# Kernel optimization log

Hardware: AMD Instinct MI355X
Metric: run time of the kernel (lower is better)

Reference implementation:

```python
import jax, jax.numpy as jnp
import numpy as np

N_NODES = 102400
N_EDGES = 1638400
NUM_GRAPHS = 128
IN_DIM = 128
HID = 128
OUT_DIM = 2
NUM_LAYERS = 3
BN_EPS = 1e-5


def setup_inputs() -> dict:
    key = jax.random.key(0)
    ks = jax.random.split(key, 12)
    x = jax.random.normal(ks[0], (N_NODES, IN_DIM), dtype=jnp.float32)
    edge_index = jax.random.randint(ks[1], (2, N_EDGES), 0, N_NODES, dtype=jnp.int64)
    # 128 graphs of 800 nodes each, sorted segment ids
    batch = jnp.repeat(jnp.arange(NUM_GRAPHS, dtype=jnp.int64), N_NODES // NUM_GRAPHS)
    s = 1.0 / np.sqrt(HID)
    W_conv = jax.random.uniform(ks[2], (NUM_LAYERS, HID, HID), jnp.float32, -s, s)
    b_conv = jnp.zeros((NUM_LAYERS, HID), jnp.float32)
    gamma = jnp.ones((NUM_LAYERS, HID), jnp.float32)
    beta = jnp.zeros((NUM_LAYERS, HID), jnp.float32)
    s2 = 1.0 / np.sqrt(3 * HID)
    W_mp1 = jax.random.uniform(ks[3], (3 * HID, 3 * HID), jnp.float32, -s2, s2)
    b_mp1 = jax.random.uniform(ks[4], (3 * HID,), jnp.float32, -s2, s2)
    W_mp2 = jax.random.uniform(ks[5], (3 * HID, OUT_DIM), jnp.float32, -s2, s2)
    b_mp2 = jax.random.uniform(ks[6], (OUT_DIM,), jnp.float32, -s2, s2)
    return {"x": x, "edge_index": edge_index, "batch": batch,
            "W_conv": W_conv, "b_conv": b_conv, "gamma": gamma, "beta": beta,
            "W_mp1": W_mp1, "b_mp1": b_mp1, "W_mp2": W_mp2, "b_mp2": b_mp2}


def _gcn_norm(edge_index, n):
    # add self loops, symmetric normalization: norm_e = deg^-1/2[src] * deg^-1/2[dst]
    loop = jnp.arange(n, dtype=edge_index.dtype)
    src = jnp.concatenate([edge_index[0], loop])
    dst = jnp.concatenate([edge_index[1], loop])
    deg = jax.ops.segment_sum(jnp.ones_like(dst, dtype=jnp.float32), dst, num_segments=n)
    dinv = jnp.where(deg > 0, jax.lax.rsqrt(deg), 0.0)
    return src, dst, dinv[src] * dinv[dst]


def reference(x, edge_index, batch, W_conv, b_conv, gamma, beta, W_mp1, b_mp1, W_mp2, b_mp2):
    n = x.shape[0]
    src, dst, norm = _gcn_norm(edge_index, n)
    for i in range(NUM_LAYERS):
        h = x @ W_conv[i]                                    # [N, HID]
        h = jax.ops.segment_sum(h[src] * norm[:, None], dst, num_segments=n) + b_conv[i]
        h = jax.nn.relu(h)
        mu = jnp.mean(h, axis=0)
        var = jnp.var(h, axis=0)                             # biased, as torch BN
        x = (h - mu) * jax.lax.rsqrt(var + BN_EPS) * gamma[i] + beta[i]
        # dropout p=0.0 -> no-op
    # readout: max pool, mean pool, first-node gather
    x1 = jax.ops.segment_max(x, batch, num_segments=NUM_GRAPHS)
    cnt = jax.ops.segment_sum(jnp.ones((n,), jnp.float32), batch, num_segments=NUM_GRAPHS)
    x2 = jax.ops.segment_sum(x, batch, num_segments=NUM_GRAPHS) / cnt[:, None]
    first_idx = jnp.searchsorted(batch, jnp.arange(NUM_GRAPHS, dtype=batch.dtype))
    x3 = x[first_idx]
    g = jnp.concatenate([x1, x2, x3], axis=1)                # [B, 3*HID]
    g = (g @ W_mp1 + b_mp1) @ W_mp2 + b_mp2
    return jax.nn.log_softmax(g, axis=1)
```

## Files before the change

kernel.cpp:

```cpp
#include <hip/hip_runtime.h>
#include <hip/hip_bf16.h>
#include <cstdint>

#define N_NODESC  102400
#define N_EDGESC  1638400
#define NUM_GRAPHS 128
#define NPG       800
#define HID       128
#define BN_EPS    1e-5f

#define NFINE 1600
#define NCOARSE 25
#define ROUND 2048

typedef short short8 __attribute__((ext_vector_type(8)));
typedef float f32x4  __attribute__((ext_vector_type(4)));
typedef unsigned long long u64;

__device__ __forceinline__ unsigned short f2bf(float f){
    union { __hip_bfloat16 h; unsigned short u; } cv;
    cv.h = __float2bfloat16(f);
    return cv.u;
}
__device__ __forceinline__ float bflo(unsigned int g){ return __uint_as_float(g << 16); }
__device__ __forceinline__ float bfhi(unsigned int g){ return __uint_as_float(g & 0xffff0000u); }
__device__ __forceinline__ float bfu(unsigned short u){ return __uint_as_float(((unsigned int)u) << 16); }

__global__ __launch_bounds__(256) void k_h1(const int* __restrict__ ei, int* __restrict__ fineCount){
    __shared__ int h[NFINE];
    int t = threadIdx.x;
    for (int i = t; i < NFINE; i += 256) h[i] = 0;
    __syncthreads();
    for (int e = blockIdx.x*256 + t; e < N_EDGESC; e += gridDim.x*256){
        int d = __builtin_nontemporal_load(&ei[N_EDGESC + e]);
        atomicAdd(&h[d >> 6], 1);
    }
    __syncthreads();
    for (int i = t; i < NFINE; i += 256) if (h[i]) atomicAdd(&fineCount[i], h[i]);
}

__global__ __launch_bounds__(256) void k_scanF(const int* __restrict__ fineCount, int* __restrict__ fineBase,
                                               int* __restrict__ fineCursor, int* __restrict__ coarseCursor){
    __shared__ int part[256];
    __shared__ int shb[NFINE];
    int t = threadIdx.x;
    int loc[7]; int s = 0;
    #pragma unroll
    for (int j = 0; j < 7; j++){
        int idx = t*7 + j;
        int v = (idx < NFINE) ? fineCount[idx] : 0;
        loc[j] = s; s += v;
    }
    part[t] = s;
    __syncthreads();
    if (t == 0){
        int run = 0;
        for (int i = 0; i < 256; i++){ int v = part[i]; part[i] = run; run += v; }
    }
    __syncthreads();
    #pragma unroll
    for (int j = 0; j < 7; j++){
        int idx = t*7 + j;
        if (idx < NFINE){
            int b = part[t] + loc[j];
            shb[idx] = b;
            fineBase[idx]   = b;
            fineCursor[idx] = b;
        }
    }
    __syncthreads();
    if (t < NCOARSE) coarseCursor[t] = shb[t*64];
}

__global__ __launch_bounds__(256) void k_binA(const int* __restrict__ ei, int* __restrict__ coarseCursor,
                                              u64* __restrict__ coarseBuf){
    __shared__ int cnt[NCOARSE], gpos[NCOARSE], baseS[NCOARSE+1];
    __shared__ u64 stage[ROUND];
    __shared__ short bkt[ROUND];
    int t = threadIdx.x;
    int chunk = blockIdx.x * ROUND;
    if (t < NCOARSE) cnt[t] = 0;
    __syncthreads();
    u64 ed[8]; int b[8], rk[8];
    #pragma unroll
    for (int j = 0; j < 8; j++){
        int e = chunk + t + j*256;
        unsigned int s = (unsigned int)__builtin_nontemporal_load(&ei[e]);
        unsigned int d = (unsigned int)__builtin_nontemporal_load(&ei[N_EDGESC + e]);
        ed[j] = ((u64)d << 32) | (u64)s;
        b[j] = (int)(d >> 12);
        rk[j] = atomicAdd(&cnt[b[j]], 1);
    }
    __syncthreads();
    if (t == 0){
        int s = 0;
        for (int i = 0; i < NCOARSE; i++){ baseS[i] = s; s += cnt[i]; }
        baseS[NCOARSE] = s;
    }
    __syncthreads();
    if (t < NCOARSE && cnt[t] > 0) gpos[t] = atomicAdd(&coarseCursor[t], cnt[t]);
    __syncthreads();
    #pragma unroll
    for (int j = 0; j < 8; j++){
        int p = baseS[b[j]] + rk[j];
        stage[p] = ed[j];
        bkt[p] = (short)b[j];
    }
    __syncthreads();
    #pragma unroll
    for (int j = 0; j < 8; j++){
        int p = t + j*256;
        int bb = bkt[p];
        coarseBuf[gpos[bb] + (p - baseS[bb])] = stage[p];
    }
}

__global__ __launch_bounds__(256) void k_binB(const u64* __restrict__ coarseBuf, const int* __restrict__ fineBase,
                                              int* __restrict__ fineCursor, u64* __restrict__ fineBuf){
    int c   = blockIdx.x >> 5;
    int sub = blockIdx.x & 31;
    int segB = fineBase[c*64];
    int segE = (c == NCOARSE-1) ? N_EDGESC : fineBase[(c+1)*64];
    __shared__ int cnt[64], gpos[64], baseS[65];
    __shared__ u64 stage[ROUND];
    __shared__ short bkt[ROUND];
    int t = threadIdx.x;
    for (int r = sub; ; r += 32){
        int base = segB + r*ROUND;
        if (base >= segE) break;
        int m = segE - base; if (m > ROUND) m = ROUND;
        if (t < 64) cnt[t] = 0;
        __syncthreads();
        u64 ed[8]; int b[8], rk[8], val[8];
        #pragma unroll
        for (int j = 0; j < 8; j++){
            int i = t + j*256;
            val[j] = (i < m);
            if (val[j]){
                ed[j] = __builtin_nontemporal_load(&coarseBuf[base + i]);
                b[j] = (int)((ed[j] >> 38) & 63);
                rk[j] = atomicAdd(&cnt[b[j]], 1);
            }
        }
        __syncthreads();
        if (t == 0){
            int s = 0;
            for (int i = 0; i < 64; i++){ baseS[i] = s; s += cnt[i]; }
            baseS[64] = s;
        }
        __syncthreads();
        if (t < 64 && cnt[t] > 0) gpos[t] = atomicAdd(&fineCursor[c*64 + t], cnt[t]);
        __syncthreads();
        #pragma unroll
        for (int j = 0; j < 8; j++){
            if (val[j]){
                int p = baseS[b[j]] + rk[j];
                stage[p] = ed[j];
                bkt[p] = (short)b[j];
            }
        }
        __syncthreads();
        int total = baseS[64];
        #pragma unroll
        for (int j = 0; j < 8; j++){
            int p = t + j*256;
            if (p < total){
                int bb = bkt[p];
                fineBuf[gpos[bb] + (p - baseS[bb])] = stage[p];
            }
        }
        __syncthreads();
    }
}

__global__ __launch_bounds__(256) void k_binC(const u64* __restrict__ fineBuf, const int* __restrict__ fineBase,
                                              const int* __restrict__ fineCount, int* __restrict__ row_ptr,
                                              float* __restrict__ dinv, int* __restrict__ srcS){
    int f = blockIdx.x, t = threadIdx.x;
    int gB = fineBase[f];
    int cntE = fineCount[f];
    __shared__ int deg[64], excl[64], cur[64];
    if (t < 64){ deg[t] = 0; cur[t] = 0; }
    __syncthreads();
    for (int i = t; i < cntE; i += 256){
        int lo = (int)((fineBuf[gB + i] >> 32) & 63);
        atomicAdd(&deg[lo], 1);
    }
    __syncthreads();
    if (t == 0){
        int s = 0;
        for (int i = 0; i < 64; i++){ excl[i] = s; s += deg[i]; }
    }
    __syncthreads();
    if (t < 64){
        row_ptr[f*64 + t] = gB + excl[t];
        dinv[f*64 + t] = rsqrtf((float)(deg[t] + 1));
    }
    if (f == 0 && t == 0) row_ptr[N_NODESC] = N_EDGESC;
    for (int i = t; i < cntE; i += 256){
        u64 ed = fineBuf[gB + i];
        int lo = (int)((ed >> 32) & 63);
        int pos = gB + excl[lo] + atomicAdd(&cur[lo], 1);
        srcS[pos] = (int)(unsigned int)(ed & 0xffffffffu);
    }
}

__global__ __launch_bounds__(256) void k_prepw0(const float* __restrict__ W, unsigned short* __restrict__ Wt,
                                                float* __restrict__ biasv){
    int idx = blockIdx.x*256 + threadIdx.x;
    int n = idx & 127, k = idx >> 7;
    Wt[n*128 + k] = f2bf(W[k*128 + n]);
    if (idx < 128) biasv[idx] = 0.f;
}

template<int F32IN>
__global__ __launch_bounds__(256) void k_gemm_mfma(const void* __restrict__ Xin,
        const unsigned short* __restrict__ Wt, const float* __restrict__ biasv,
        const float* __restrict__ dinv, unsigned short* __restrict__ H){
    int l   = threadIdx.x & 63;
    int wid = threadIdx.x >> 6;
    int R   = blockIdx.x*64 + wid*16;
    int r0  = l & 15;
    int kg  = l >> 4;
    short8 a[4];
    if (F32IN){
        const float* X = (const float*)Xin;
        #pragma unroll
        for (int kk = 0; kk < 4; kk++){
            const float* p = X + (size_t)(R + r0)*HID + kk*32 + kg*8;
            float4 u = *(const float4*)p;
            float4 v = *(const float4*)(p + 4);
            short8 tt;
            tt[0]=(short)f2bf(u.x); tt[1]=(short)f2bf(u.y); tt[2]=(short)f2bf(u.z); tt[3]=(short)f2bf(u.w);
            tt[4]=(short)f2bf(v.x); tt[5]=(short)f2bf(v.y); tt[6]=(short)f2bf(v.z); tt[7]=(short)f2bf(v.w);
            a[kk] = tt;
        }
    } else {
        const unsigned short* X = (const unsigned short*)Xin;
        #pragma unroll
        for (int kk = 0; kk < 4; kk++)
            a[kk] = *(const short8*)(X + (size_t)(R + r0)*HID + kk*32 + kg*8);
    }
    f32x4 acc[8];
    #pragma unroll
    for (int i = 0; i < 8; i++) acc[i] = (f32x4)(0.f);
    #pragma unroll
    for (int kk = 0; kk < 4; kk++){
        #pragma unroll
        for (int nf = 0; nf < 8; nf++){
            short8 b = *(const short8*)(Wt + (size_t)(nf*16 + r0)*HID + kk*32 + kg*8);
            acc[nf] = __builtin_amdgcn_mfma_f32_16x16x32_bf16(a[kk], b, acc[nf], 0, 0, 0);
        }
    }
    float bv[8];
    #pragma unroll
    for (int nf = 0; nf < 8; nf++) bv[nf] = biasv[nf*16 + r0];
    #pragma unroll
    for (int r = 0; r < 4; r++){
        int row = R + kg*4 + r;
        float di = dinv[row];
        #pragma unroll
        for (int nf = 0; nf < 8; nf++)
            H[(size_t)row*HID + nf*16 + r0] = f2bf(di * (acc[nf][r] + bv[nf]));
    }
}

__global__ __launch_bounds__(256) void k_agg(const unsigned int* __restrict__ Hb, const int* __restrict__ row_ptr,
                                             const int* __restrict__ srcS, const float* __restrict__ dinv,
                                             const float* __restrict__ bconv,
                                             unsigned int* __restrict__ OUT, float* __restrict__ sum,
                                             float* __restrict__ sumsq){
    int lane = threadIdx.x & 63;
    int w    = threadIdx.x >> 6;
    int wave = blockIdx.x*4 + w;
    int nw   = gridDim.x*4;
    float2 bc = ((const float2*)bconv)[lane];
    float sx0 = 0.f, sx1 = 0.f, sq0 = 0.f, sq1 = 0.f;
    const int NPAIR = N_NODESC/2;
    for (int pb = wave; pb < NPAIR; pb += nw){
        int nA = 2*pb, nB = 2*pb + 1;
        int eA  = row_ptr[nA], e1A = row_ptr[nA+1], e1B = row_ptr[nB+1];
        int eB  = e1A;
        unsigned int gsA = Hb[(size_t)nA*64 + lane];
        unsigned int gsB = Hb[(size_t)nB*64 + lane];
        float axA = bflo(gsA), ayA = bfhi(gsA);
        float axB = bflo(gsB), ayB = bfhi(gsB);
        while (eA + 4 <= e1A && eB + 4 <= e1B){
            int4 sa = *(const int4*)(srcS + eA);
            int4 sb = *(const int4*)(srcS + eB);
            unsigned int g0 = Hb[(size_t)sa.x*64 + lane];
            unsigned int g1 = Hb[(size_t)sa.y*64 + lane];
            unsigned int g2 = Hb[(size_t)sa.z*64 + lane];
            unsigned int g3 = Hb[(size_t)sa.w*64 + lane];
            unsigned int h0 = Hb[(size_t)sb.x*64 + lane];
            unsigned int h1 = Hb[(size_t)sb.y*64 + lane];
            unsigned int h2 = Hb[(size_t)sb.z*64 + lane];
            unsigned int h3 = Hb[(size_t)sb.w*64 + lane];
            axA += bflo(g0); ayA += bfhi(g0);
            axA += bflo(g1); ayA += bfhi(g1);
            axA += bflo(g2); ayA += bfhi(g2);
            axA += bflo(g3); ayA += bfhi(g3);
            axB += bflo(h0); ayB += bfhi(h0);
            axB += bflo(h1); ayB += bfhi(h1);
            axB += bflo(h2); ayB += bfhi(h2);
            axB += bflo(h3); ayB += bfhi(h3);
            eA += 4; eB += 4;
        }
        for (; eA + 4 <= e1A; eA += 4){
            int4 sa = *(const int4*)(srcS + eA);
            unsigned int g0 = Hb[(size_t)sa.x*64 + lane];
            unsigned int g1 = Hb[(size_t)sa.y*64 + lane];
            unsigned int g2 = Hb[(size_t)sa.z*64 + lane];
            unsigned int g3 = Hb[(size_t)sa.w*64 + lane];
            axA += bflo(g0); ayA += bfhi(g0);
            axA += bflo(g1); ayA += bfhi(g1);
            axA += bflo(g2); ayA += bfhi(g2);
            axA += bflo(g3); ayA += bfhi(g3);
        }
        for (; eB + 4 <= e1B; eB += 4){
            int4 sb = *(const int4*)(srcS + eB);
            unsigned int h0 = Hb[(size_t)sb.x*64 + lane];
            unsigned int h1 = Hb[(size_t)sb.y*64 + lane];
            unsigned int h2 = Hb[(size_t)sb.z*64 + lane];
            unsigned int h3 = Hb[(size_t)sb.w*64 + lane];
            axB += bflo(h0); ayB += bfhi(h0);
            axB += bflo(h1); ayB += bfhi(h1);
            axB += bflo(h2); ayB += bfhi(h2);
            axB += bflo(h3); ayB += bfhi(h3);
        }
        while (eA < e1A || eB < e1B){
            unsigned int g = 0, h = 0;
            int doA = (eA < e1A), doB = (eB < e1B);
            if (doA) g = Hb[(size_t)srcS[eA]*64 + lane];
            if (doB) h = Hb[(size_t)srcS[eB]*64 + lane];
            if (doA){ axA += bflo(g); ayA += bfhi(g); eA++; }
            if (doB){ axB += bflo(h); ayB += bfhi(h); eB++; }
        }
        float dA = dinv[nA], dB = dinv[nB];
        axA = fmaxf(fmaf(axA, dA, bc.x), 0.f);
        ayA = fmaxf(fmaf(ayA, dA, bc.y), 0.f);
        axB = fmaxf(fmaf(axB, dB, bc.x), 0.f);
        ayB = fmaxf(fmaf(ayB, dB, bc.y), 0.f);
        unsigned int oA = ((unsigned int)f2bf(ayA) << 16) | (unsigned int)f2bf(axA);
        unsigned int oB = ((unsigned int)f2bf(ayB) << 16) | (unsigned int)f2bf(axB);
        __builtin_nontemporal_store(oA, &OUT[(size_t)nA*64 + lane]);
        __builtin_nontemporal_store(oB, &OUT[(size_t)nB*64 + lane]);
        sx0 += axA + axB; sq0 += axA*axA + axB*axB;
        sx1 += ayA + ayB; sq1 += ayA*ayA + ayB*ayB;
    }
    __shared__ float shs[4][128];
    __shared__ float shq[4][128];
    shs[w][2*lane]   = sx0; shs[w][2*lane+1] = sx1;
    shq[w][2*lane]   = sq0; shq[w][2*lane+1] = sq1;
    __syncthreads();
    int t = threadIdx.x;
    if (t < 128){
        atomicAdd(&sum[t],   shs[0][t] + shs[1][t] + shs[2][t] + shs[3][t]);
        atomicAdd(&sumsq[t], shq[0][t] + shq[1][t] + shq[2][t] + shq[3][t]);
    }
}

__global__ __launch_bounds__(128) void k_fin1(const float* __restrict__ sum, const float* __restrict__ sumsq,
                                              const float* __restrict__ gamma, const float* __restrict__ beta,
                                              const float* __restrict__ Wnext, float* __restrict__ A,
                                              float* __restrict__ B, float* __restrict__ biasv, int hasNext){
    __shared__ float Bsh[128];
    int c = threadIdx.x;
    const float invN = 1.0f / (float)N_NODESC;
    float mu  = sum[c] * invN;
    float var = sumsq[c] * invN - mu*mu;
    float is  = rsqrtf(var + BN_EPS);
    float a = is * gamma[c];
    float b = beta[c] - mu * a;
    A[c] = a; B[c] = b; Bsh[c] = b;
    __syncthreads();
    if (hasNext){
        float bv = 0.f;
        for (int k = 0; k < 128; k++)
            bv = fmaf(Bsh[k], Wnext[k*128 + c], bv);
        biasv[c] = bv;
    }
}

__global__ __launch_bounds__(256) void k_fin2(const float* __restrict__ A, const float* __restrict__ Wnext,
                                              unsigned short* __restrict__ WpT){
    int idx = blockIdx.x*256 + threadIdx.x;
    int c = idx >> 7, k = idx & 127;
    WpT[c*128 + k] = f2bf(A[k] * Wnext[k*128 + c]);
}

__global__ __launch_bounds__(512) void k_poolmlp(const unsigned short* __restrict__ X, const float* __restrict__ A,
                                                 const float* __restrict__ B, const float* __restrict__ W1,
                                                 const float* __restrict__ b1, const float* __restrict__ W2,
                                                 const float* __restrict__ b2, float* __restrict__ out){
    __shared__ float shm[4][128];
    __shared__ float shsm[4][128];
    __shared__ float row[384];
    __shared__ float t1[384];
    __shared__ float r0[512], r1[512];
    int t = threadIdx.x, gr = blockIdx.x;
    int c = t & 127, sl = t >> 7;
    float a = A[c], b = B[c];
    const unsigned short* base = X + ((size_t)gr*NPG + sl*200)*HID;
    float mx = -1e30f, sm = 0.f;
    for (int i = 0; i < 200; i++){
        float v = fmaf(bfu(base[(size_t)i*HID + c]), a, b);
        mx = fmaxf(mx, v); sm += v;
    }
    shm[sl][c] = mx; shsm[sl][c] = sm;
    if (sl == 0) row[256 + c] = fmaf(bfu(base[c]), a, b);
    __syncthreads();
    if (t < 128){
        float m = fmaxf(fmaxf(shm[0][t], shm[1][t]), fmaxf(shm[2][t], shm[3][t]));
        float s = shsm[0][t] + shsm[1][t] + shsm[2][t] + shsm[3][t];
        row[t]       = m;
        row[128 + t] = s * (1.0f/(float)NPG);
    }
    __syncthreads();
    if (t < 384){
        float acc = b1[t];
        for (int k = 0; k < 384; k++) acc = fmaf(row[k], W1[(size_t)k*384 + t], acc);
        t1[t] = acc;
    }
    __syncthreads();
    float p0 = 0.f, p1 = 0.f;
    if (t < 384){ float v = t1[t]; p0 = v*W2[t*2]; p1 = v*W2[t*2+1]; }
    r0[t] = p0; r1[t] = p1; __syncthreads();
    for (int off = 256; off > 0; off >>= 1){
        if (t < off){ r0[t] += r0[t+off]; r1[t] += r1[t+off]; }
        __syncthreads();
    }
    if (t == 0){
        float o0 = r0[0] + b2[0], o1 = r1[0] + b2[1];
        float m = fmaxf(o0, o1);
        float lse = m + logf(expf(o0 - m) + expf(o1 - m));
        out[gr*2 + 0] = o0 - lse;
        out[gr*2 + 1] = o1 - lse;
    }
}

extern "C" void kernel_launch(void* const* d_in, const int* in_sizes, int n_in,
                              void* d_out, int out_size, void* d_ws, size_t ws_size,
                              hipStream_t stream){
    const float* x     = (const float*)d_in[0];
    const int*   ei    = (const int*)d_in[1];
    const float* Wconv = (const float*)d_in[3];
    const float* bconv = (const float*)d_in[4];
    const float* gamma = (const float*)d_in[5];
    const float* beta  = (const float*)d_in[6];
    const float* W1    = (const float*)d_in[7];
    const float* b1    = (const float*)d_in[8];
    const float* W2    = (const float*)d_in[9];
    const float* b2    = (const float*)d_in[10];
    float* out = (float*)d_out;

    char* p = (char*)d_ws;
    size_t off = 0;
    auto alloc = [&](size_t bytes)->char* {
        char* r = p + off; off += (bytes + 255) & ~(size_t)255; return r;
    };
    unsigned short* buf1 = (unsigned short*)alloc((size_t)N_NODESC*HID*2);
    unsigned short* buf2 = (unsigned short*)alloc((size_t)N_NODESC*HID*2);
    u64*  coarseBuf  = (u64*)  alloc((size_t)N_EDGESC*8);
    u64*  fineBuf    = (u64*)  alloc((size_t)N_EDGESC*8);
    int*   srcS      = (int*)  alloc((size_t)N_EDGESC*4);
    int*   row_ptr   = (int*)  alloc((size_t)(N_NODESC+1)*4);
    float* dinv      = (float*)alloc((size_t)N_NODESC*4);
    int*   fineCount = (int*)  alloc(NFINE*4);
    int*   fineBase  = (int*)  alloc(NFINE*4);
    int*   fineCursor= (int*)  alloc(NFINE*4);
    int*   coarseCursor=(int*) alloc(NCOARSE*4);
    float* stats   = (float*)alloc(3*2*128*4);
    float* AB      = (float*)alloc(3*2*128*4);
    unsigned short* Wt0 = (unsigned short*)alloc(128*128*2);
    unsigned short* WpT = (unsigned short*)alloc(128*128*2);
    float* biasv   = (float*)alloc(512);
    (void)ws_size; (void)in_sizes; (void)n_in; (void)out_size;

    hipMemsetAsync(fineCount, 0, NFINE*4, stream);
    hipMemsetAsync(stats, 0, 3*2*128*4, stream);

    k_h1   <<<256, 256, 0, stream>>>(ei, fineCount);
    k_scanF<<<1,   256, 0, stream>>>(fineCount, fineBase, fineCursor, coarseCursor);
    k_binA <<<N_EDGESC/ROUND, 256, 0, stream>>>(ei, coarseCursor, coarseBuf);
    k_binB <<<NCOARSE*32, 256, 0, stream>>>(coarseBuf, fineBase, fineCursor, fineBuf);
    k_binC <<<NFINE, 256, 0, stream>>>(fineBuf, fineBase, fineCount, row_ptr, dinv, srcS);
    k_prepw0<<<64, 256, 0, stream>>>(Wconv, Wt0, biasv);

    for (int l = 0; l < 3; l++){
        if (l == 0)
            k_gemm_mfma<1><<<N_NODESC/64, 256, 0, stream>>>((const void*)x, Wt0, biasv, dinv, buf1);
        else
            k_gemm_mfma<0><<<N_NODESC/64, 256, 0, stream>>>((const void*)buf2, WpT, biasv, dinv, buf1);
        k_agg<<<2048, 256, 0, stream>>>((const unsigned int*)buf1, row_ptr, srcS, dinv,
                                        bconv + l*HID, (unsigned int*)buf2,
                                        stats + l*256, stats + l*256 + 128);
        k_fin1<<<1, 128, 0, stream>>>(stats + l*256, stats + l*256 + 128,
                                      gamma + l*HID, beta + l*HID,
                                      Wconv + (size_t)(l+1 < 3 ? l+1 : 0)*HID*HID,
                                      AB + l*256, AB + l*256 + 128,
                                      biasv, (l < 2) ? 1 : 0);
        if (l < 2)
            k_fin2<<<64, 256, 0, stream>>>(AB + l*256,
                                           Wconv + (size_t)(l+1)*HID*HID, WpT);
    }
    k_poolmlp<<<NUM_GRAPHS, 512, 0, stream>>>(buf2, AB + 2*256, AB + 2*256 + 128,
                                              W1, b1, W2, b2, out);
}
```

Baseline: 531.1 us.

## Fold memsets into prep kernel, merge finalize kernels, nontemporal index loads

Replaces the two hipMemsetAsync calls by zeroing fineCount and stats inside k_prepw0, which now runs first. k_fin1 and k_fin2 are merged into one single-block k_finalize that also writes the scaled transposed weights, so each layer launches one kernel fewer. The aggregation kernel's row_ptr and srcS reads become nontemporal loads, and its grid doubles to 4096 blocks. Together these cut launch count and cache pollution, but the merged finalize does 16K weight writes from only 128 threads, with strided stores.

```diff
diff --git a/kernel.cpp b/kernel.cpp
--- a/kernel.cpp
+++ b/kernel.cpp
@@ -15,6 +15,7 @@
 
 typedef short short8 __attribute__((ext_vector_type(8)));
 typedef float f32x4  __attribute__((ext_vector_type(4)));
+typedef int   intx4  __attribute__((ext_vector_type(4)));
 typedef unsigned long long u64;
 
 __device__ __forceinline__ unsigned short f2bf(float f){
@@ -206,11 +207,14 @@
 }
 
 __global__ __launch_bounds__(256) void k_prepw0(const float* __restrict__ W, unsigned short* __restrict__ Wt,
+                                                int* __restrict__ fineCount, float* __restrict__ stats,
                                                 float* __restrict__ biasv){
     int idx = blockIdx.x*256 + threadIdx.x;
     int n = idx & 127, k = idx >> 7;
     Wt[n*128 + k] = f2bf(W[k*128 + n]);
-    if (idx < 128) biasv[idx] = 0.f;
+    if (idx < NFINE) fineCount[idx] = 0;
+    else if (idx < NFINE + 768) stats[idx - NFINE] = 0.f;
+    else if (idx < NFINE + 768 + 128) biasv[idx - NFINE - 768] = 0.f;
 }
 
 template<int F32IN>
@@ -279,23 +283,25 @@
     const int NPAIR = N_NODESC/2;
     for (int pb = wave; pb < NPAIR; pb += nw){
         int nA = 2*pb, nB = 2*pb + 1;
-        int eA  = row_ptr[nA], e1A = row_ptr[nA+1], e1B = row_ptr[nB+1];
+        int eA  = __builtin_nontemporal_load(&row_ptr[nA]);
+        int e1A = __builtin_nontemporal_load(&row_ptr[nA+1]);
+        int e1B = __builtin_nontemporal_load(&row_ptr[nB+1]);
         int eB  = e1A;
         unsigned int gsA = Hb[(size_t)nA*64 + lane];
         unsigned int gsB = Hb[(size_t)nB*64 + lane];
         float axA = bflo(gsA), ayA = bfhi(gsA);
         float axB = bflo(gsB), ayB = bfhi(gsB);
         while (eA + 4 <= e1A && eB + 4 <= e1B){
-            int4 sa = *(const int4*)(srcS + eA);
-            int4 sb = *(const int4*)(srcS + eB);
-            unsigned int g0 = Hb[(size_t)sa.x*64 + lane];
-            unsigned int g1 = Hb[(size_t)sa.y*64 + lane];
-            unsigned int g2 = Hb[(size_t)sa.z*64 + lane];
-            unsigned int g3 = Hb[(size_t)sa.w*64 + lane];
-            unsigned int h0 = Hb[(size_t)sb.x*64 + lane];
-            unsigned int h1 = Hb[(size_t)sb.y*64 + lane];
-            unsigned int h2 = Hb[(size_t)sb.z*64 + lane];
-            unsigned int h3 = Hb[(size_t)sb.w*64 + lane];
+            intx4 sa = __builtin_nontemporal_load((const intx4*)(srcS + eA));
+            intx4 sb = __builtin_nontemporal_load((const intx4*)(srcS + eB));
+            unsigned int g0 = Hb[(size_t)sa[0]*64 + lane];
+            unsigned int g1 = Hb[(size_t)sa[1]*64 + lane];
+            unsigned int g2 = Hb[(size_t)sa[2]*64 + lane];
+            unsigned int g3 = Hb[(size_t)sa[3]*64 + lane];
+            unsigned int h0 = Hb[(size_t)sb[0]*64 + lane];
+            unsigned int h1 = Hb[(size_t)sb[1]*64 + lane];
+            unsigned int h2 = Hb[(size_t)sb[2]*64 + lane];
+            unsigned int h3 = Hb[(size_t)sb[3]*64 + lane];
             axA += bflo(g0); ayA += bfhi(g0);
             axA += bflo(g1); ayA += bfhi(g1);
             axA += bflo(g2); ayA += bfhi(g2);
@@ -307,22 +313,22 @@
             eA += 4; eB += 4;
         }
         for (; eA + 4 <= e1A; eA += 4){
-            int4 sa = *(const int4*)(srcS + eA);
-            unsigned int g0 = Hb[(size_t)sa.x*64 + lane];
-            unsigned int g1 = Hb[(size_t)sa.y*64 + lane];
-            unsigned int g2 = Hb[(size_t)sa.z*64 + lane];
-            unsigned int g3 = Hb[(size_t)sa.w*64 + lane];
+            intx4 sa = __builtin_nontemporal_load((const intx4*)(srcS + eA));
+            unsigned int g0 = Hb[(size_t)sa[0]*64 + lane];
+            unsigned int g1 = Hb[(size_t)sa[1]*64 + lane];
+            unsigned int g2 = Hb[(size_t)sa[2]*64 + lane];
+            unsigned int g3 = Hb[(size_t)sa[3]*64 + lane];
             axA += bflo(g0); ayA += bfhi(g0);
             axA += bflo(g1); ayA += bfhi(g1);
             axA += bflo(g2); ayA += bfhi(g2);
             axA += bflo(g3); ayA += bfhi(g3);
         }
         for (; eB + 4 <= e1B; eB += 4){
-            int4 sb = *(const int4*)(srcS + eB);
-            unsigned int h0 = Hb[(size_t)sb.x*64 + lane];
-            unsigned int h1 = Hb[(size_t)sb.y*64 + lane];
-            unsigned int h2 = Hb[(size_t)sb.z*64 + lane];
-            unsigned int h3 = Hb[(size_t)sb.w*64 + lane];
+            intx4 sb = __builtin_nontemporal_load((const intx4*)(srcS + eB));
+            unsigned int h0 = Hb[(size_t)sb[0]*64 + lane];
+            unsigned int h1 = Hb[(size_t)sb[1]*64 + lane];
+            unsigned int h2 = Hb[(size_t)sb[2]*64 + lane];
+            unsigned int h3 = Hb[(size_t)sb[3]*64 + lane];
             axB += bflo(h0); ayB += bfhi(h0);
             axB += bflo(h1); ayB += bfhi(h1);
             axB += bflo(h2); ayB += bfhi(h2);
@@ -331,8 +337,8 @@
         while (eA < e1A || eB < e1B){
             unsigned int g = 0, h = 0;
             int doA = (eA < e1A), doB = (eB < e1B);
-            if (doA) g = Hb[(size_t)srcS[eA]*64 + lane];
-            if (doB) h = Hb[(size_t)srcS[eB]*64 + lane];
+            if (doA) g = Hb[(size_t)__builtin_nontemporal_load(&srcS[eA])*64 + lane];
+            if (doB) h = Hb[(size_t)__builtin_nontemporal_load(&srcS[eB])*64 + lane];
             if (doA){ axA += bflo(g); ayA += bfhi(g); eA++; }
             if (doB){ axB += bflo(h); ayB += bfhi(h); eB++; }
         }
@@ -360,11 +366,12 @@
     }
 }
 
-__global__ __launch_bounds__(128) void k_fin1(const float* __restrict__ sum, const float* __restrict__ sumsq,
-                                              const float* __restrict__ gamma, const float* __restrict__ beta,
-                                              const float* __restrict__ Wnext, float* __restrict__ A,
-                                              float* __restrict__ B, float* __restrict__ biasv, int hasNext){
-    __shared__ float Bsh[128];
+__global__ __launch_bounds__(128) void k_finalize(const float* __restrict__ sum, const float* __restrict__ sumsq,
+                                                  const float* __restrict__ gamma, const float* __restrict__ beta,
+                                                  const float* __restrict__ Wnext, float* __restrict__ A,
+                                                  float* __restrict__ B, unsigned short* __restrict__ WpT,
+                                                  float* __restrict__ biasv, int hasNext){
+    __shared__ float Ash[128], Bsh[128];
     int c = threadIdx.x;
     const float invN = 1.0f / (float)N_NODESC;
     float mu  = sum[c] * invN;
@@ -372,21 +379,17 @@
     float is  = rsqrtf(var + BN_EPS);
     float a = is * gamma[c];
     float b = beta[c] - mu * a;
-    A[c] = a; B[c] = b; Bsh[c] = b;
+    A[c] = a; B[c] = b; Ash[c] = a; Bsh[c] = b;
     __syncthreads();
     if (hasNext){
         float bv = 0.f;
-        for (int k = 0; k < 128; k++)
-            bv = fmaf(Bsh[k], Wnext[k*128 + c], bv);
+        for (int k = 0; k < 128; k++){
+            float w = Wnext[k*128 + c];
+            WpT[c*128 + k] = f2bf(Ash[k] * w);
+            bv = fmaf(Bsh[k], w, bv);
+        }
         biasv[c] = bv;
     }
-}
-
-__global__ __launch_bounds__(256) void k_fin2(const float* __restrict__ A, const float* __restrict__ Wnext,
-                                              unsigned short* __restrict__ WpT){
-    int idx = blockIdx.x*256 + threadIdx.x;
-    int c = idx >> 7, k = idx & 127;
-    WpT[c*128 + k] = f2bf(A[k] * Wnext[k*128 + c]);
 }
 
 __global__ __launch_bounds__(512) void k_poolmlp(const unsigned short* __restrict__ X, const float* __restrict__ A,
@@ -477,32 +480,27 @@
     float* biasv   = (float*)alloc(512);
     (void)ws_size; (void)in_sizes; (void)n_in; (void)out_size;
 
-    hipMemsetAsync(fineCount, 0, NFINE*4, stream);
-    hipMemsetAsync(stats, 0, 3*2*128*4, stream);
+    k_prepw0<<<64, 256, 0, stream>>>(Wconv, Wt0, fineCount, stats, biasv);
 
     k_h1   <<<256, 256, 0, stream>>>(ei, fineCount);
     k_scanF<<<1,   256, 0, stream>>>(fineCount, fineBase, fineCursor, coarseCursor);
     k_binA <<<N_EDGESC/ROUND, 256, 0, stream>>>(ei, coarseCursor, coarseBuf);
     k_binB <<<NCOARSE*32, 256, 0, stream>>>(coarseBuf, fineBase, fineCursor, fineBuf);
     k_binC <<<NFINE, 256, 0, stream>>>(fineBuf, fineBase, fineCount, row_ptr, dinv, srcS);
-    k_prepw0<<<64, 256, 0, stream>>>(Wconv, Wt0, biasv);
 
     for (int l = 0; l < 3; l++){
         if (l == 0)
             k_gemm_mfma<1><<<N_NODESC/64, 256, 0, stream>>>((const void*)x, Wt0, biasv, dinv, buf1);
         else
             k_gemm_mfma<0><<<N_NODESC/64, 256, 0, stream>>>((const void*)buf2, WpT, biasv, dinv, buf1);
-        k_agg<<<2048, 256, 0, stream>>>((const unsigned int*)buf1, row_ptr, srcS, dinv,
+        k_agg<<<4096, 256, 0, stream>>>((const unsigned int*)buf1, row_ptr, srcS, dinv,
                                         bconv + l*HID, (unsigned int*)buf2,
                                         stats + l*256, stats + l*256 + 128);
-        k_fin1<<<1, 128, 0, stream>>>(stats + l*256, stats + l*256 + 128,
-                                      gamma + l*HID, beta + l*HID,
-                                      Wconv + (size_t)(l+1 < 3 ? l+1 : 0)*HID*HID,
-                                      AB + l*256, AB + l*256 + 128,
-                                      biasv, (l < 2) ? 1 : 0);
-        if (l < 2)
-            k_fin2<<<64, 256, 0, stream>>>(AB + l*256,
-                                           Wconv + (size_t)(l+1)*HID*HID, WpT);
+        k_finalize<<<1, 128, 0, stream>>>(stats + l*256, stats + l*256 + 128,
+                                          gamma + l*HID, beta + l*HID,
+                                          Wconv + (size_t)(l+1 < 3 ? l+1 : 0)*HID*HID,
+                                          AB + l*256, AB + l*256 + 128,
+                                          WpT, biasv, (l < 2) ? 1 : 0);
     }
     k_poolmlp<<<NUM_GRAPHS, 512, 0, stream>>>(buf2, AB + 2*256, AB + 2*256 + 128,
                                               W1, b1, W2, b2, out);
```

New measurement: 628.5 us. 18.3% more time.
